# Kernel tuning notes

Measured on AMD Instinct MI355X. Metric: run time of the kernel, lower is better.

The kernel has to match this reference:

```python
import jax, jax.numpy as jnp
import numpy as np


def setup_inputs() -> dict:
    key = jax.random.key(0)
    k1, k2, k3, k4, k5 = jax.random.split(key, 5)
    B, N, M, D = 16, 8192, 8192, 256
    emb = jax.random.normal(k1, (B, M, D), dtype=jnp.float32)
    pts = jax.random.normal(k2, (B, N, 5), dtype=jnp.float32)
    num = jax.random.randint(k3, (B,), 1, M + 1)
    indeces = jax.random.randint(k4, (B, M), 0, N)
    W = jax.random.normal(k5, (4, D), dtype=jnp.float32) * (1.414 / np.sqrt(4 + D))
    image_shape = jnp.array([B, 3, 768, 1024], dtype=jnp.int64)  # (b, c, H, W)
    return {"emb": emb, "num": num, "pts": pts, "indeces": indeces,
            "image_shape": image_shape, "W": W}


def reference(emb, num, pts, indeces, image_shape, W):
    height = image_shape[2].astype(jnp.float32)
    width = image_shape[3].astype(jnp.float32)
    # normalize_keypoints: center at image center, scale by 0.7*max(W,H)
    size = jnp.stack([width, height])                      # [2] (w, h)
    center = size / 2.0
    scaling = jnp.max(size) * 0.7
    upts = (pts[..., :2] - center) / scaling               # [B,N,2]
    # normalize_angle: (angle - 45) / (180*0.7)
    uangle = (pts[..., 4:5] - 45.0) / (180.0 * 0.7)        # [B,N,1]
    # normalize_len: scale by 0.7*diag, center at half that
    diag = jnp.sqrt(width * width + height * height)
    lscale = diag * 0.7
    ulen = (pts[..., 3:4] - lscale / 2.0) / lscale         # [B,N,1]
    feat = jnp.concatenate([upts, uangle, ulen], axis=-1)  # [B,N,4]
    pose_feature = jnp.einsum("bnf,fd->bnd", feat, W)      # [B,N,D]
    # per-batch gather of pose_feature rows, added to first num[b] emb slots
    gathered = jnp.take_along_axis(pose_feature, indeces[..., None], axis=1)  # [B,M,D]
    slot = jnp.arange(emb.shape[1])[None, :]               # [1,M]
    mask = (slot < num[:, None])[..., None]                # [B,M,1]
    return emb + jnp.where(mask, gathered, 0.0)
```

## Files before the change

### kernel.cpp

```cpp
#include <hip/hip_runtime.h>


__global__ __launch_bounds__(256) void PosFeatureLayer_83416854823346_kernel(
    const float* __restrict__ emb,
    const int* __restrict__ num,
    const float* __restrict__ pts,
    const int* __restrict__ indeces,
    const int* __restrict__ image_shape,
    const float* __restrict__ W,
    float* __restrict__ out,
    int B, int M, int N, int D)
{
    const int lane = threadIdx.x & 63;
    const int wave = threadIdx.x >> 6;
    const int m = blockIdx.x * 4 + wave;
    const int b = blockIdx.y;
    if (m >= M) return;

    const float h = (float)image_shape[2];
    const float w = (float)image_shape[3];
    const float scaling = fmaxf(w, h) * 0.7f;
    const float inv_s   = 1.0f / scaling;
    const float cx = w * 0.5f, cy = h * 0.5f;
    const float lscale = sqrtf(w * w + h * h) * 0.7f;
    const float inv_l  = 1.0f / lscale;
    const float inv_a  = 1.0f / (180.0f * 0.7f);

    float f0 = 0.f, f1 = 0.f, f2 = 0.f, f3 = 0.f;
    if (m < num[b]) {
        const int idx = indeces[(long long)b * M + m];
        const float* p = pts + ((long long)b * N + (long long)idx) * 5;
        f0 = (p[0] - cx) * inv_s;
        f1 = (p[1] - cy) * inv_s;
        f2 = (p[4] - 45.0f) * inv_a;
        f3 = (p[3] - lscale * 0.5f) * inv_l;
    }

    const long long rowoff = ((long long)b * M + m) * (long long)D;
    for (int d0 = lane * 4; d0 < D; d0 += 64 * 4) {
        const float4 w0 = *(const float4*)(W + 0 * D + d0);
        const float4 w1 = *(const float4*)(W + 1 * D + d0);
        const float4 w2 = *(const float4*)(W + 2 * D + d0);
        const float4 w3 = *(const float4*)(W + 3 * D + d0);
        const float4 e  = *(const float4*)(emb + rowoff + d0);
        float4 r;
        r.x = e.x + f0 * w0.x + f1 * w1.x + f2 * w2.x + f3 * w3.x;
        r.y = e.y + f0 * w0.y + f1 * w1.y + f2 * w2.y + f3 * w3.y;
        r.z = e.z + f0 * w0.z + f1 * w1.z + f2 * w2.z + f3 * w3.z;
        r.w = e.w + f0 * w0.w + f1 * w1.w + f2 * w2.w + f3 * w3.w;
        *(float4*)(out + rowoff + d0) = r;
    }
}

extern "C" void kernel_launch(void* const* d_in, const int* in_sizes, int n_in,
                              void* d_out, int out_size, void* d_ws, size_t ws_size,
                              hipStream_t stream) {
    (void)n_in; (void)d_ws; (void)ws_size;
    const float* emb  = (const float*)d_in[0];
    const int*   num  = (const int*)d_in[1];
    const float* pts  = (const float*)d_in[2];
    const int*   idx  = (const int*)d_in[3];
    const int*   ishp = (const int*)d_in[4];
    const float* Wm   = (const float*)d_in[5];
    float*       out  = (float*)d_out;

    const int B = in_sizes[1];
    const int D = in_sizes[5] / 4;
    const int M = (int)((long long)in_sizes[3] / B);
    const int N = (int)((long long)in_sizes[2] / ((long long)B * 5));
    (void)out_size;

    dim3 block(256);
    dim3 grid((M + 3) / 4, B);
    hipLaunchKernelGGL(PosFeatureLayer_83416854823346_kernel, grid, block, 0, stream,
                       emb, num, pts, idx, ishp, Wm, out, B, M, N, D);
}
```

Baseline: 56.03 us.

## Process eight rows per wave with shuffled index/point loads for D=256

Adds a D=256 specialized kernel in which each wave handles eight consecutive rows instead of one. W is loaded once per wave and reused across those rows. Indices and point coordinates are fetched cooperatively by a few lanes and broadcast with shuffles, and all eight emb rows are loaded up front to raise memory-level parallelism. This cuts redundant W, index and point loads and launches eight times fewer blocks, at the cost of more registers per thread and lower wave count.

Result: faster. 48.12 us (-14.1%).

```diff
diff --git a/kernel.cpp b/kernel.cpp
--- a/kernel.cpp
+++ b/kernel.cpp
@@ -1,7 +1,9 @@
 #include <hip/hip_runtime.h>
 
 
-__global__ __launch_bounds__(256) void PosFeatureLayer_83416854823346_kernel(
+#define DD 256
+
+__global__ __launch_bounds__(256) void posfeat_d256_kernel(
     const float* __restrict__ emb,
     const int* __restrict__ num,
     const float* __restrict__ pts,
@@ -9,23 +11,94 @@
     const int* __restrict__ image_shape,
     const float* __restrict__ W,
     float* __restrict__ out,
-    int B, int M, int N, int D)
+    int B, int M, int N)
+{
+    const int lane = threadIdx.x & 63;
+    const int wave = threadIdx.x >> 6;
+    const int b = blockIdx.y;
+    const int base_m = (blockIdx.x * 4 + wave) * 8;
+    if (base_m >= M) return;
+
+    const float h = (float)image_shape[2];
+    const float w = (float)image_shape[3];
+    const float inv_s  = 1.0f / (fmaxf(w, h) * 0.7f);
+    const float cx = w * 0.5f, cy = h * 0.5f;
+    const float lscale = sqrtf(w * w + h * h) * 0.7f;
+    const float inv_l  = 1.0f / lscale;
+    const float half_l = lscale * 0.5f;
+    const float inv_a  = 1.0f / 126.0f;
+
+    const int d0 = lane * 4;
+    const float4 w0 = *(const float4*)(W + 0 * DD + d0);
+    const float4 w1 = *(const float4*)(W + 1 * DD + d0);
+    const float4 w2 = *(const float4*)(W + 2 * DD + d0);
+    const float4 w3 = *(const float4*)(W + 3 * DD + d0);
+
+    const int nb = num[b];
+
+    int idxv = -1;
+    if (lane < 8) {
+        const int m = base_m + lane;
+        if (m < M && m < nb) idxv = indeces[(long long)b * M + m];
+    }
+    float pv = 0.f;
+    {
+        const int r = lane / 5, c = lane - r * 5;
+        const int ir = __shfl(idxv, r);
+        if (lane < 40 && ir >= 0)
+            pv = pts[((long long)b * N + ir) * 5 + c];
+    }
+
+    const long long baseoff = ((long long)b * M + base_m) * DD + d0;
+    const int nrows = (M - base_m < 8) ? (M - base_m) : 8;
+
+    float4 e[8];
+    #pragma unroll
+    for (int r = 0; r < 8; ++r)
+        if (r < nrows) e[r] = *(const float4*)(emb + baseoff + (long long)r * DD);
+
+    #pragma unroll
+    for (int r = 0; r < 8; ++r) {
+        if (r >= nrows) continue;
+        const int   ir = __shfl(idxv, r);
+        const float p0 = __shfl(pv, r * 5 + 0);
+        const float p1 = __shfl(pv, r * 5 + 1);
+        const float p3 = __shfl(pv, r * 5 + 3);
+        const float p4 = __shfl(pv, r * 5 + 4);
+        float f0 = 0.f, f1 = 0.f, f2 = 0.f, f3 = 0.f;
+        if (ir >= 0) {
+            f0 = (p0 - cx) * inv_s;
+            f1 = (p1 - cy) * inv_s;
+            f2 = (p4 - 45.0f) * inv_a;
+            f3 = (p3 - half_l) * inv_l;
+        }
+        float4 o;
+        o.x = e[r].x + f0 * w0.x + f1 * w1.x + f2 * w2.x + f3 * w3.x;
+        o.y = e[r].y + f0 * w0.y + f1 * w1.y + f2 * w2.y + f3 * w3.y;
+        o.z = e[r].z + f0 * w0.z + f1 * w1.z + f2 * w2.z + f3 * w3.z;
+        o.w = e[r].w + f0 * w0.w + f1 * w1.w + f2 * w2.w + f3 * w3.w;
+        *(float4*)(out + baseoff + (long long)r * DD) = o;
+    }
+}
+
+__global__ __launch_bounds__(256) void posfeat_generic_kernel(
+    const float* __restrict__ emb, const int* __restrict__ num,
+    const float* __restrict__ pts, const int* __restrict__ indeces,
+    const int* __restrict__ image_shape, const float* __restrict__ W,
+    float* __restrict__ out, int B, int M, int N, int D)
 {
     const int lane = threadIdx.x & 63;
     const int wave = threadIdx.x >> 6;
     const int m = blockIdx.x * 4 + wave;
     const int b = blockIdx.y;
     if (m >= M) return;
-
     const float h = (float)image_shape[2];
     const float w = (float)image_shape[3];
-    const float scaling = fmaxf(w, h) * 0.7f;
-    const float inv_s   = 1.0f / scaling;
+    const float inv_s = 1.0f / (fmaxf(w, h) * 0.7f);
     const float cx = w * 0.5f, cy = h * 0.5f;
     const float lscale = sqrtf(w * w + h * h) * 0.7f;
-    const float inv_l  = 1.0f / lscale;
-    const float inv_a  = 1.0f / (180.0f * 0.7f);
-
+    const float inv_l = 1.0f / lscale;
+    const float inv_a = 1.0f / 126.0f;
     float f0 = 0.f, f1 = 0.f, f2 = 0.f, f3 = 0.f;
     if (m < num[b]) {
         const int idx = indeces[(long long)b * M + m];
@@ -35,27 +108,26 @@
         f2 = (p[4] - 45.0f) * inv_a;
         f3 = (p[3] - lscale * 0.5f) * inv_l;
     }
-
     const long long rowoff = ((long long)b * M + m) * (long long)D;
-    for (int d0 = lane * 4; d0 < D; d0 += 64 * 4) {
-        const float4 w0 = *(const float4*)(W + 0 * D + d0);
-        const float4 w1 = *(const float4*)(W + 1 * D + d0);
-        const float4 w2 = *(const float4*)(W + 2 * D + d0);
-        const float4 w3 = *(const float4*)(W + 3 * D + d0);
-        const float4 e  = *(const float4*)(emb + rowoff + d0);
+    for (int dd = lane * 4; dd < D; dd += 64 * 4) {
+        const float4 w0 = *(const float4*)(W + 0 * D + dd);
+        const float4 w1 = *(const float4*)(W + 1 * D + dd);
+        const float4 w2 = *(const float4*)(W + 2 * D + dd);
+        const float4 w3 = *(const float4*)(W + 3 * D + dd);
+        const float4 e  = *(const float4*)(emb + rowoff + dd);
         float4 r;
         r.x = e.x + f0 * w0.x + f1 * w1.x + f2 * w2.x + f3 * w3.x;
         r.y = e.y + f0 * w0.y + f1 * w1.y + f2 * w2.y + f3 * w3.y;
         r.z = e.z + f0 * w0.z + f1 * w1.z + f2 * w2.z + f3 * w3.z;
         r.w = e.w + f0 * w0.w + f1 * w1.w + f2 * w2.w + f3 * w3.w;
-        *(float4*)(out + rowoff + d0) = r;
+        *(float4*)(out + rowoff + dd) = r;
     }
 }
 
 extern "C" void kernel_launch(void* const* d_in, const int* in_sizes, int n_in,
                               void* d_out, int out_size, void* d_ws, size_t ws_size,
                               hipStream_t stream) {
-    (void)n_in; (void)d_ws; (void)ws_size;
+    (void)n_in; (void)d_ws; (void)ws_size; (void)out_size;
     const float* emb  = (const float*)d_in[0];
     const int*   num  = (const int*)d_in[1];
     const float* pts  = (const float*)d_in[2];
@@ -68,10 +140,16 @@
     const int D = in_sizes[5] / 4;
     const int M = (int)((long long)in_sizes[3] / B);
     const int N = (int)((long long)in_sizes[2] / ((long long)B * 5));
-    (void)out_size;
 
-    dim3 block(256);
-    dim3 grid((M + 3) / 4, B);
-    hipLaunchKernelGGL(PosFeatureLayer_83416854823346_kernel, grid, block, 0, stream,
-                       emb, num, pts, idx, ishp, Wm, out, B, M, N, D);
+    if (D == 256) {
+        dim3 block(256);
+        dim3 grid((M + 31) / 32, B);
+        hipLaunchKernelGGL(posfeat_d256_kernel, grid, block, 0, stream,
+                           emb, num, pts, idx, ishp, Wm, out, B, M, N);
+    } else {
+        dim3 block(256);
+        dim3 grid((M + 3) / 4, B);
+        hipLaunchKernelGGL(posfeat_generic_kernel, grid, block, 0, stream,
+                           emb, num, pts, idx, ishp, Wm, out, B, M, N, D);
+    }
 }
```
